# Kernel tuning notes

Hardware: AMD Instinct MI355X
Metric: run time of the kernel (lower is better)

The kernel has to match this reference:

```python
import jax, jax.numpy as jnp
import numpy as np

B, S, D = 32, 4096, 256
MASK_FILL = 1e-9  # note: mask is applied AFTER softmax, matching the torch code


def setup_inputs() -> dict:
    key = jax.random.key(0)
    k1, k2, k3, k4 = jax.random.split(key, 4)
    return {
        "key": jax.random.normal(k1, (B, S, D), dtype=jnp.float32),
        "value": jax.random.normal(k2, (B, S, D), dtype=jnp.float32),
        "token": jax.random.normal(k3, (B, D), dtype=jnp.float32),
        "lens": jax.random.randint(k4, (B,), 1, S, dtype=jnp.int64),
    }


def reference(key, value, token, lens):
    # energy: [B, S] = bmm(key, token[...,None]) squeezed
    energy = jnp.einsum("bsd,bd->bs", key, token)
    w = jax.nn.softmax(energy, axis=1)
    # unusual semantics: masked positions are set to 1e-9 AFTER softmax
    mask = jnp.arange(key.shape[1])[None, :] >= lens[:, None]  # [B, S]
    w = jnp.where(mask, jnp.asarray(MASK_FILL, w.dtype), w)
    # context: [B, D] = bmm(value^T, w[...,None]) squeezed
    context = jnp.einsum("bsd,bs->bd", value, w)
    return context
```

## Files before the change

### kernel.cpp

```cpp
#include <hip/hip_runtime.h>
#include <cmath>

#define S 4096
#define D 256
#define BATCH 32
#define CHUNK 64
#define NCHUNK (S / CHUNK)
#define SHIFT 40.0f

__global__ __launch_bounds__(256, 4)
void fused_pass_kernel(const float* __restrict__ key,
                       const float* __restrict__ value,
                       const float* __restrict__ token,
                       const void* __restrict__ lens,
                       float* __restrict__ Ap,
                       float* __restrict__ Lp) {
    const int b     = blockIdx.x >> 6;
    const int chunk = blockIdx.x & (NCHUNK - 1);
    const int t     = threadIdx.x;
    const int wid   = t >> 6;
    const int lane  = t & 63;
    const int grp   = lane >> 4;
    const int sl    = lane & 15;

    __shared__ float wa_s[4][16];
    __shared__ float redA[4][D];
    __shared__ float redL[4];

    const int* p32 = (const int*)lens;
    const int len = (p32[1] == 0) ? (int)(((const long long*)lens)[b]) : p32[b];

    const int s0 = chunk * CHUNK + wid * 16;

    const float* tb = token + b * D + sl * 16;
    const float4 tk0 = *reinterpret_cast<const float4*>(tb + 0);
    const float4 tk1 = *reinterpret_cast<const float4*>(tb + 4);
    const float4 tk2 = *reinterpret_cast<const float4*>(tb + 8);
    const float4 tk3 = *reinterpret_cast<const float4*>(tb + 12);

    const float* kbase = key + ((size_t)b * S + s0) * D + sl * 16;
    float Lacc = 0.f;

    float4 kA0, kA1, kA2, kA3, kB0, kB1, kB2, kB3;

#define KLOAD(P0, P1, P2, P3, g)                                              \
    {                                                                         \
        const float* kr_ = kbase + (size_t)(((g) * 4 + grp) * D);             \
        P0 = *reinterpret_cast<const float4*>(kr_ + 0);                       \
        P1 = *reinterpret_cast<const float4*>(kr_ + 4);                       \
        P2 = *reinterpret_cast<const float4*>(kr_ + 8);                       \
        P3 = *reinterpret_cast<const float4*>(kr_ + 12);                      \
    }

#define KCOMP(P0, P1, P2, P3, g)                                              \
    {                                                                         \
        float d0_ = P0.x * tk0.x + P0.y * tk0.y + P0.z * tk0.z + P0.w * tk0.w;\
        float d1_ = P1.x * tk1.x + P1.y * tk1.y + P1.z * tk1.z + P1.w * tk1.w;\
        float d2_ = P2.x * tk2.x + P2.y * tk2.y + P2.z * tk2.z + P2.w * tk2.w;\
        float d3_ = P3.x * tk3.x + P3.y * tk3.y + P3.z * tk3.z + P3.w * tk3.w;\
        float p_ = (d0_ + d1_) + (d2_ + d3_);                                 \
        p_ += __shfl_xor(p_, 1);                                              \
        p_ += __shfl_xor(p_, 2);                                              \
        p_ += __shfl_xor(p_, 4);                                              \
        p_ += __shfl_xor(p_, 8);                                              \
        const float wE_ = __expf(p_ - SHIFT);                                 \
        if (sl == 0) {                                                        \
            Lacc += wE_;                                                      \
            wa_s[wid][(g) * 4 + grp] =                                        \
                (s0 + (g) * 4 + grp < len) ? wE_ : 0.f;                       \
        }                                                                     \
    }

    KLOAD(kA0, kA1, kA2, kA3, 0)
    KLOAD(kB0, kB1, kB2, kB3, 1)
    __builtin_amdgcn_sched_barrier(0);
    KCOMP(kA0, kA1, kA2, kA3, 0)
    KLOAD(kA0, kA1, kA2, kA3, 2)
    KCOMP(kB0, kB1, kB2, kB3, 1)
    KLOAD(kB0, kB1, kB2, kB3, 3)
    KCOMP(kA0, kA1, kA2, kA3, 2)
    KCOMP(kB0, kB1, kB2, kB3, 3)

    float4 accA = make_float4(0.f, 0.f, 0.f, 0.f);
    if (s0 < len) {
        const float* vbase = value + ((size_t)b * S + s0) * D + lane * 4;
        float4 vA0, vA1, vA2, vA3, vB0, vB1, vB2, vB3;

#define VLOAD(P0, P1, P2, P3, r0)                                             \
    {                                                                         \
        P0 = *reinterpret_cast<const float4*>(vbase + (size_t)((r0) + 0) * D);\
        P1 = *reinterpret_cast<const float4*>(vbase + (size_t)((r0) + 1) * D);\
        P2 = *reinterpret_cast<const float4*>(vbase + (size_t)((r0) + 2) * D);\
        P3 = *reinterpret_cast<const float4*>(vbase + (size_t)((r0) + 3) * D);\
    }

#define VCOMP(P0, P1, P2, P3, r0)                                             \
    {                                                                         \
        const float w0_ = wa_s[wid][(r0) + 0];                                \
        const float w1_ = wa_s[wid][(r0) + 1];                                \
        const float w2_ = wa_s[wid][(r0) + 2];                                \
        const float w3_ = wa_s[wid][(r0) + 3];                                \
        accA.x += w0_ * P0.x; accA.y += w0_ * P0.y;                           \
        accA.z += w0_ * P0.z; accA.w += w0_ * P0.w;                           \
        accA.x += w1_ * P1.x; accA.y += w1_ * P1.y;                           \
        accA.z += w1_ * P1.z; accA.w += w1_ * P1.w;                           \
        accA.x += w2_ * P2.x; accA.y += w2_ * P2.y;                           \
        accA.z += w2_ * P2.z; accA.w += w2_ * P2.w;                           \
        accA.x += w3_ * P3.x; accA.y += w3_ * P3.y;                           \
        accA.z += w3_ * P3.z; accA.w += w3_ * P3.w;                           \
    }

        VLOAD(vA0, vA1, vA2, vA3, 0)
        VLOAD(vB0, vB1, vB2, vB3, 4)
        __builtin_amdgcn_sched_barrier(0);
        VCOMP(vA0, vA1, vA2, vA3, 0)
        VLOAD(vA0, vA1, vA2, vA3, 8)
        VCOMP(vB0, vB1, vB2, vB3, 4)
        VLOAD(vB0, vB1, vB2, vB3, 12)
        VCOMP(vA0, vA1, vA2, vA3, 8)
        VCOMP(vB0, vB1, vB2, vB3, 12)
    }

    #pragma unroll
    for (int off = 32; off > 0; off >>= 1) Lacc += __shfl_xor(Lacc, off);
    if (lane == 0) redL[wid] = Lacc;
    *reinterpret_cast<float4*>(&redA[wid][lane * 4]) = accA;
    __syncthreads();

    const float sA = redA[0][t] + redA[1][t] + redA[2][t] + redA[3][t];
    Ap[(b * NCHUNK + chunk) * D + t] = sA;
    if (t == 0) Lp[b * NCHUNK + chunk] = redL[0] + redL[1] + redL[2] + redL[3];
}

__global__ void finalize_kernel(const float* __restrict__ Ap,
                                const float* __restrict__ Lp,
                                float* __restrict__ out) {
    const int b = blockIdx.x;
    const int t = threadIdx.x;
    float l = 0.f;
    #pragma unroll
    for (int c = 0; c < NCHUNK; ++c) l += Lp[b * NCHUNK + c];
    float a = 0.f;
    #pragma unroll 16
    for (int c = 0; c < NCHUNK; ++c) a += Ap[(b * NCHUNK + c) * D + t];
    out[b * D + t] = a / l;
}

extern "C" void kernel_launch(void* const* d_in, const int* in_sizes, int n_in,
                              void* d_out, int out_size, void* d_ws, size_t ws_size,
                              hipStream_t stream) {
    const float* key   = (const float*)d_in[0];
    const float* value = (const float*)d_in[1];
    const float* token = (const float*)d_in[2];
    const void*  lens  = d_in[3];
    float* out = (float*)d_out;

    float* Ap = (float*)d_ws;
    float* Lp = Ap + BATCH * NCHUNK * D;

    fused_pass_kernel<<<BATCH * NCHUNK, 256, 0, stream>>>(
        key, value, token, lens, Ap, Lp);
    finalize_kernel<<<BATCH, D, 0, stream>>>(Ap, Lp, out);
}
```

Measured before the change: 40.07 us.

## Interleave key and value loads per group with smaller blocks and batch-major chunk order

Each group of four rows now issues its key and value loads together, then computes the scores and accumulates the values, instead of finishing all key work before starting the value pass. Blocks shrink to 128 threads covering 32 rows. Block index ordering changes so consecutive blocks belong to different batches, and the finalize kernel now reduces twice as many partials. The aim is more memory-level parallelism and better load balance across batches with different lengths, at the cost of a larger partial-sum buffer and a shallower prefetch pipeline inside each wave.

```diff
diff --git a/kernel.cpp b/kernel.cpp
--- a/kernel.cpp
+++ b/kernel.cpp
@@ -4,33 +4,34 @@
 #define S 4096
 #define D 256
 #define BATCH 32
-#define CHUNK 64
+#define CHUNK 32
 #define NCHUNK (S / CHUNK)
 #define SHIFT 40.0f
 
-__global__ __launch_bounds__(256, 4)
+__global__ __launch_bounds__(128, 8)
 void fused_pass_kernel(const float* __restrict__ key,
                        const float* __restrict__ value,
                        const float* __restrict__ token,
                        const void* __restrict__ lens,
                        float* __restrict__ Ap,
                        float* __restrict__ Lp) {
-    const int b     = blockIdx.x >> 6;
-    const int chunk = blockIdx.x & (NCHUNK - 1);
+    const int chunk = blockIdx.x >> 5;
+    const int b     = blockIdx.x & (BATCH - 1);
     const int t     = threadIdx.x;
     const int wid   = t >> 6;
     const int lane  = t & 63;
     const int grp   = lane >> 4;
     const int sl    = lane & 15;
 
-    __shared__ float wa_s[4][16];
-    __shared__ float redA[4][D];
-    __shared__ float redL[4];
+    __shared__ float wa_s[2][16];
+    __shared__ float redA[2][D];
+    __shared__ float redL[2];
 
     const int* p32 = (const int*)lens;
     const int len = (p32[1] == 0) ? (int)(((const long long*)lens)[b]) : p32[b];
 
-    const int s0 = chunk * CHUNK + wid * 16;
+    const int s0    = chunk * CHUNK + wid * 16;
+    const bool alive = s0 < len;
 
     const float* tb = token + b * D + sl * 16;
     const float4 tk0 = *reinterpret_cast<const float4*>(tb + 0);
@@ -38,26 +39,33 @@
     const float4 tk2 = *reinterpret_cast<const float4*>(tb + 8);
     const float4 tk3 = *reinterpret_cast<const float4*>(tb + 12);
 
-    const float* kbase = key + ((size_t)b * S + s0) * D + sl * 16;
-    float Lacc = 0.f;
+    const float* kb = key   + ((size_t)b * S + s0) * D;
+    const float* vb = value + ((size_t)b * S + s0) * D + lane * 4;
 
-    float4 kA0, kA1, kA2, kA3, kB0, kB1, kB2, kB3;
+    float4 acc  = make_float4(0.f, 0.f, 0.f, 0.f);
+    float  Lacc = 0.f;
 
-#define KLOAD(P0, P1, P2, P3, g)                                              \
+#define GROUP(g)                                                              \
     {                                                                         \
-        const float* kr_ = kbase + (size_t)(((g) * 4 + grp) * D);             \
-        P0 = *reinterpret_cast<const float4*>(kr_ + 0);                       \
-        P1 = *reinterpret_cast<const float4*>(kr_ + 4);                       \
-        P2 = *reinterpret_cast<const float4*>(kr_ + 8);                       \
-        P3 = *reinterpret_cast<const float4*>(kr_ + 12);                      \
-    }
-
-#define KCOMP(P0, P1, P2, P3, g)                                              \
-    {                                                                         \
-        float d0_ = P0.x * tk0.x + P0.y * tk0.y + P0.z * tk0.z + P0.w * tk0.w;\
-        float d1_ = P1.x * tk1.x + P1.y * tk1.y + P1.z * tk1.z + P1.w * tk1.w;\
-        float d2_ = P2.x * tk2.x + P2.y * tk2.y + P2.z * tk2.z + P2.w * tk2.w;\
-        float d3_ = P3.x * tk3.x + P3.y * tk3.y + P3.z * tk3.z + P3.w * tk3.w;\
+          \
+        const float* kr_ = kb + (size_t)((g) * 4 + grp) * D + sl * 16;        \
+        const float4 k0_ = *reinterpret_cast<const float4*>(kr_ + 0);         \
+        const float4 k1_ = *reinterpret_cast<const float4*>(kr_ + 4);         \
+        const float4 k2_ = *reinterpret_cast<const float4*>(kr_ + 8);         \
+        const float4 k3_ = *reinterpret_cast<const float4*>(kr_ + 12);        \
+        float4 v0_, v1_, v2_, v3_;                                            \
+        if (alive) {                                                          \
+            v0_ = *reinterpret_cast<const float4*>(vb + (size_t)((g)*4+0)*D); \
+            v1_ = *reinterpret_cast<const float4*>(vb + (size_t)((g)*4+1)*D); \
+            v2_ = *reinterpret_cast<const float4*>(vb + (size_t)((g)*4+2)*D); \
+            v3_ = *reinterpret_cast<const float4*>(vb + (size_t)((g)*4+3)*D); \
+        }                                                                     \
+        __builtin_amdgcn_sched_barrier(0);       \
+        \
+        float d0_ = k0_.x * tk0.x + k0_.y * tk0.y + k0_.z * tk0.z + k0_.w * tk0.w; \
+        float d1_ = k1_.x * tk1.x + k1_.y * tk1.y + k1_.z * tk1.z + k1_.w * tk1.w; \
+        float d2_ = k2_.x * tk2.x + k2_.y * tk2.y + k2_.z * tk2.z + k2_.w * tk2.w; \
+        float d3_ = k3_.x * tk3.x + k3_.y * tk3.y + k3_.z * tk3.z + k3_.w * tk3.w; \
         float p_ = (d0_ + d1_) + (d2_ + d3_);                                 \
         p_ += __shfl_xor(p_, 1);                                              \
         p_ += __shfl_xor(p_, 2);                                              \
@@ -69,67 +77,41 @@
             wa_s[wid][(g) * 4 + grp] =                                        \
                 (s0 + (g) * 4 + grp < len) ? wE_ : 0.f;                       \
         }                                                                     \
+          \
+        if (alive) {                                                          \
+            const float w0_ = wa_s[wid][(g) * 4 + 0];                         \
+            const float w1_ = wa_s[wid][(g) * 4 + 1];                         \
+            const float w2_ = wa_s[wid][(g) * 4 + 2];                         \
+            const float w3_ = wa_s[wid][(g) * 4 + 3];                         \
+            acc.x += w0_ * v0_.x; acc.y += w0_ * v0_.y;                       \
+            acc.z += w0_ * v0_.z; acc.w += w0_ * v0_.w;                       \
+            acc.x += w1_ * v1_.x; acc.y += w1_ * v1_.y;                       \
+            acc.z += w1_ * v1_.z; acc.w += w1_ * v1_.w;                       \
+            acc.x += w2_ * v2_.x; acc.y += w2_ * v2_.y;                       \
+            acc.z += w2_ * v2_.z; acc.w += w2_ * v2_.w;                       \
+            acc.x += w3_ * v3_.x; acc.y += w3_ * v3_.y;                       \
+            acc.z += w3_ * v3_.z; acc.w += w3_ * v3_.w;                       \
+        }                                                                     \
     }
 
-    KLOAD(kA0, kA1, kA2, kA3, 0)
-    KLOAD(kB0, kB1, kB2, kB3, 1)
-    __builtin_amdgcn_sched_barrier(0);
-    KCOMP(kA0, kA1, kA2, kA3, 0)
-    KLOAD(kA0, kA1, kA2, kA3, 2)
-    KCOMP(kB0, kB1, kB2, kB3, 1)
-    KLOAD(kB0, kB1, kB2, kB3, 3)
-    KCOMP(kA0, kA1, kA2, kA3, 2)
-    KCOMP(kB0, kB1, kB2, kB3, 3)
-
-    float4 accA = make_float4(0.f, 0.f, 0.f, 0.f);
-    if (s0 < len) {
-        const float* vbase = value + ((size_t)b * S + s0) * D + lane * 4;
-        float4 vA0, vA1, vA2, vA3, vB0, vB1, vB2, vB3;
-
-#define VLOAD(P0, P1, P2, P3, r0)                                             \
-    {                                                                         \
-        P0 = *reinterpret_cast<const float4*>(vbase + (size_t)((r0) + 0) * D);\
-        P1 = *reinterpret_cast<const float4*>(vbase + (size_t)((r0) + 1) * D);\
-        P2 = *reinterpret_cast<const float4*>(vbase + (size_t)((r0) + 2) * D);\
-        P3 = *reinterpret_cast<const float4*>(vbase + (size_t)((r0) + 3) * D);\
-    }
-
-#define VCOMP(P0, P1, P2, P3, r0)                                             \
-    {                                                                         \
-        const float w0_ = wa_s[wid][(r0) + 0];                                \
-        const float w1_ = wa_s[wid][(r0) + 1];                                \
-        const float w2_ = wa_s[wid][(r0) + 2];                                \
-        const float w3_ = wa_s[wid][(r0) + 3];                                \
-        accA.x += w0_ * P0.x; accA.y += w0_ * P0.y;                           \
-        accA.z += w0_ * P0.z; accA.w += w0_ * P0.w;                           \
-        accA.x += w1_ * P1.x; accA.y += w1_ * P1.y;                           \
-        accA.z += w1_ * P1.z; accA.w += w1_ * P1.w;                           \
-        accA.x += w2_ * P2.x; accA.y += w2_ * P2.y;                           \
-        accA.z += w2_ * P2.z; accA.w += w2_ * P2.w;                           \
-        accA.x += w3_ * P3.x; accA.y += w3_ * P3.y;                           \
-        accA.z += w3_ * P3.z; accA.w += w3_ * P3.w;                           \
-    }
-
-        VLOAD(vA0, vA1, vA2, vA3, 0)
-        VLOAD(vB0, vB1, vB2, vB3, 4)
-        __builtin_amdgcn_sched_barrier(0);
-        VCOMP(vA0, vA1, vA2, vA3, 0)
-        VLOAD(vA0, vA1, vA2, vA3, 8)
-        VCOMP(vB0, vB1, vB2, vB3, 4)
-        VLOAD(vB0, vB1, vB2, vB3, 12)
-        VCOMP(vA0, vA1, vA2, vA3, 8)
-        VCOMP(vB0, vB1, vB2, vB3, 12)
-    }
+    GROUP(0)
+    GROUP(1)
+    GROUP(2)
+    GROUP(3)
+#undef GROUP
 
     #pragma unroll
     for (int off = 32; off > 0; off >>= 1) Lacc += __shfl_xor(Lacc, off);
     if (lane == 0) redL[wid] = Lacc;
-    *reinterpret_cast<float4*>(&redA[wid][lane * 4]) = accA;
+    *reinterpret_cast<float4*>(&redA[wid][lane * 4]) = acc;
     __syncthreads();
 
-    const float sA = redA[0][t] + redA[1][t] + redA[2][t] + redA[3][t];
-    Ap[(b * NCHUNK + chunk) * D + t] = sA;
-    if (t == 0) Lp[b * NCHUNK + chunk] = redL[0] + redL[1] + redL[2] + redL[3];
+    const float sA0 = redA[0][t]       + redA[1][t];
+    const float sA1 = redA[0][t + 128] + redA[1][t + 128];
+    float* apb = Ap + (size_t)(b * NCHUNK + chunk) * D;
+    apb[t]       = sA0;
+    apb[t + 128] = sA1;
+    if (t == 0) Lp[b * NCHUNK + chunk] = redL[0] + redL[1];
 }
 
 __global__ void finalize_kernel(const float* __restrict__ Ap,
@@ -138,11 +120,11 @@
     const int b = blockIdx.x;
     const int t = threadIdx.x;
     float l = 0.f;
-    #pragma unroll
+    #pragma unroll 16
     for (int c = 0; c < NCHUNK; ++c) l += Lp[b * NCHUNK + c];
     float a = 0.f;
     #pragma unroll 16
-    for (int c = 0; c < NCHUNK; ++c) a += Ap[(b * NCHUNK + c) * D + t];
+    for (int c = 0; c < NCHUNK; ++c) a += Ap[(size_t)(b * NCHUNK + c) * D + t];
     out[b * D + t] = a / l;
 }
 
@@ -158,7 +140,7 @@
     float* Ap = (float*)d_ws;
     float* Lp = Ap + BATCH * NCHUNK * D;
 
-    fused_pass_kernel<<<BATCH * NCHUNK, 256, 0, stream>>>(
+    fused_pass_kernel<<<BATCH * NCHUNK, 128, 0, stream>>>(
         key, value, token, lens, Ap, Lp);
     finalize_kernel<<<BATCH, D, 0, stream>>>(Ap, Lp, out);
 }
```

After: 61.72 us. 1.54x slower.
